# Performance work log

Hardware: AMD Instinct MI355X
Metric: run time of the kernel (lower is better)

The kernel has to match this reference:

```python
import jax, jax.numpy as jnp
import numpy as np
import math

B, S, D = 4, 512, 2048
NH, DEG = 8, 4            # chebyshev heads / degree
HD = D // NH              # 256
AH = 16                   # attention heads
AHD = D // AH             # 128
W = 512                   # local attention window
BASE_LR = 0.005

def rmsnorm(x, w, eps=1e-6):
    return x * jax.lax.rsqrt(jnp.mean(x * x, axis=-1, keepdims=True) + eps) * w

def cheby_rkv(xn, coeffs, momentum, gate, ema):
    # Chebyshev spectral read + EMA/TTT coefficient update (apply_cheby_rkv_v10)
    Bb, Ss, Dd = xn.shape
    u = xn.reshape(Bb, Ss, NH, HD)
    z = jnp.tanh(u.mean(-1))                       # (B,S,NH) in [-1,1]
    Ts = [jnp.ones_like(z), z]
    for _ in range(DEG - 2):
        Ts.append(2.0 * z * Ts[-1] - Ts[-2])       # Chebyshev recurrence
    T = jnp.stack(Ts[:DEG], axis=-1)               # (B,S,NH,DEG)
    out = jnp.einsum('bshk,bhkd->bshd', T, coeffs).reshape(Bb, Ss, Dd)
    grad = jnp.einsum('bshk,bshd->bhkd', T, u) / Ss
    mom = ema * momentum + (1.0 - ema) * grad
    coeffs_new = coeffs + BASE_LR * gate[:, :, None, None] * mom
    return out, coeffs_new, mom

def local_attention(q, k, v):
    # q,k,v: (B,H,S,hd); causal attention within a sliding window of W
    Bb, H, Ss, hd = q.shape
    nc = Ss // W
    q = q.reshape(Bb, H, nc, W, hd)
    k = k.reshape(Bb, H, nc, W, hd)
    v = v.reshape(Bb, H, nc, W, hd)
    kprev = jnp.concatenate([jnp.zeros_like(k[:, :, :1]), k[:, :, :-1]], axis=2)
    vprev = jnp.concatenate([jnp.zeros_like(v[:, :, :1]), v[:, :, :-1]], axis=2)
    kk = jnp.concatenate([kprev, k], axis=3)       # (B,H,nc,2W,hd)
    vv = jnp.concatenate([vprev, v], axis=3)
    qi = jnp.arange(W)
    kj = jnp.arange(2 * W)
    causal = (kj[None, :] - W) <= qi[:, None]      # (W,2W)
    chunk_ok = (jnp.arange(nc)[:, None, None] > 0) | (kj[None, None, :] >= W)
    mask = causal[None] & chunk_ok                 # (nc,W,2W)
    scores = jnp.einsum('bhnqd,bhnkd->bhnqk', q, kk) / math.sqrt(hd)
    scores = jnp.where(mask[None, None], scores, -1e9)
    attn = jax.nn.softmax(scores, axis=-1)
    o = jnp.einsum('bhnqk,bhnkd->bhnqd', attn, vv)
    return o.reshape(Bb, H, Ss, hd)

def _forward(x, w_in, wg1, bg1, wg2, bg2, wc1, bc1, wc2, bc2,
             wq, wk, wv, wo, w_nc, w_ns, w_fgv, w_np, w_out):
    Bb, Ss, Dd = x.shape
    xn = rmsnorm(x, w_in)
    x_mean = xn.mean(axis=1)                       # (B,D)
    # coeff init (cheby_state is None): MLP + spectral 1/(k+1) scaling
    h = jax.nn.silu(x_mean @ wc1 + bc1)
    coeff_raw = h @ wc2 + bc2
    kidx = jnp.arange(DEG, dtype=jnp.float32)
    spectral_scale = (0.1 / (kidx + 1.0)).reshape(1, 1, DEG, 1)
    coeffs = coeff_raw.reshape(Bb, NH, DEG, HD) * spectral_scale
    momentum = jnp.zeros_like(coeffs)
    # complexity gate (GatedComplexityPredictor)
    g = jax.nn.silu(x_mean @ wg1 + bg1)
    gate_global = jax.nn.sigmoid(g @ wg2 + bg2)    # (B,1)
    # EMA momentum schedule: total_tokens_seen = S after this call
    progress = min(Ss / 1e8, 1.0)
    ema = 0.7 + 0.5 * (0.9 - 0.7) * (1.0 + math.cos(progress * math.pi))
    cheby_out, coeffs, momentum = cheby_rkv(xn, coeffs, momentum, gate_global, ema)
    # SLR: windowed local attention, keys/values conditioned on cheby output
    kv_src = xn + cheby_out
    q = (xn @ wq).reshape(Bb, Ss, AH, AHD).transpose(0, 2, 1, 3)
    k = (kv_src @ wk).reshape(Bb, Ss, AH, AHD).transpose(0, 2, 1, 3)
    v = (kv_src @ wv).reshape(Bb, Ss, AH, AHD).transpose(0, 2, 1, 3)
    slr = local_attention(q, k, v).transpose(0, 2, 1, 3).reshape(Bb, Ss, Dd) @ wo
    # gated SwiGLU-style fusion of the two paths
    h1 = rmsnorm(cheby_out, w_nc)
    h2 = rmsnorm(slr, w_ns)
    gv = jnp.concatenate([h1, h2], axis=-1) @ w_fgv
    gate, value = gv[..., :Dd], gv[..., Dd:]
    fused = rmsnorm(jax.nn.silu(gate) * value, w_np)
    return x + fused @ w_out

def setup_inputs() -> dict:
    key = jax.random.key(0)
    ks = jax.random.split(key, 12)
    s = 0.02
    return {
        'x': jax.random.normal(ks[0], (B, S, D), jnp.float32),
        'w_in': jnp.ones((D,), jnp.float32),
        'wg1': jax.random.normal(ks[1], (D, D // 4), jnp.float32) * s,
        'bg1': jnp.zeros((D // 4,), jnp.float32),
        'wg2': jax.random.normal(ks[2], (D // 4, 1), jnp.float32) * s,
        'bg2': jnp.zeros((1,), jnp.float32),
        'wc1': jax.random.normal(ks[3], (D, D // 4), jnp.float32) * s,
        'bc1': jnp.zeros((D // 4,), jnp.float32),
        'wc2': jax.random.normal(ks[4], (D // 4, NH * DEG * HD), jnp.float32) * s,
        'bc2': jnp.zeros((NH * DEG * HD,), jnp.float32),
        'wq': jax.random.normal(ks[5], (D, D), jnp.float32) * s,
        'wk': jax.random.normal(ks[6], (D, D), jnp.float32) * s,
        'wv': jax.random.normal(ks[7], (D, D), jnp.float32) * s,
        'wo': jax.random.normal(ks[8], (D, D), jnp.float32) * s,
        'w_nc': jnp.ones((D,), jnp.float32),
        'w_ns': jnp.ones((D,), jnp.float32),
        'w_fgv': jax.random.normal(ks[9], (2 * D, 2 * D), jnp.float32) * s,
        'w_np': jnp.ones((D,), jnp.float32),
        'w_out': jax.random.normal(ks[10], (D, D), jnp.float32) * s,
    }

def reference(x, w_in, wg1, bg1, wg2, bg2, wc1, bc1, wc2, bc2,
              wq, wk, wv, wo, w_nc, w_ns, w_fgv, w_np, w_out):
    return _forward(x, w_in, wg1, bg1, wg2, bg2, wc1, bc1, wc2, bc2,
                    wq, wk, wv, wo, w_nc, w_ns, w_fgv, w_np, w_out)
```

## Files before the change

### kernel.cpp

```cpp
#include <hip/hip_runtime.h>
#include <hip/hip_bf16.h>
#include <math.h>

#define Bz 4
#define Sz 512
#define Dz 2048
#define NHz 8
#define DEGz 4
#define HDz 256
#define AHz 16
#define AHDz 128
#define SCALE_ATT 0.08838834764831845f

typedef __attribute__((ext_vector_type(8))) short short8;
typedef __attribute__((ext_vector_type(4))) float f32x4;

#define AS1 __attribute__((address_space(1)))
#define AS3 __attribute__((address_space(3)))

__device__ inline void gload16(const void* g, void* l) {
    __builtin_amdgcn_global_load_lds((const AS1 void*)g, (AS3 void*)l, 16, 0, 0);
}

struct GOp {
    const void* A; const void* B; void* C; const float* add;
    long long sAb, sAh, sBb, sBh, sCb, sCh;
    int K, lda, ldb, ldc, nbh, gx, gy, flags, tileEnd;
};
struct GArgs { int n; GOp op[6]; };

__global__ __launch_bounds__(256) void gemm_multi(GArgs ga) {
    __shared__ unsigned short As[2 * 128 * 32];
    __shared__ unsigned short Bs[2 * 128 * 32];

    int tid = blockIdx.x;
    int oi = 0;
    while (tid >= ga.op[oi].tileEnd) ++oi;
    GOp o = ga.op[oi];
    int local = tid - (oi ? ga.op[oi - 1].tileEnd : 0);
    int t = threadIdx.x;

    if (o.flags & 32) {
        const float* src = (const float*)o.A;
        __hip_bfloat16* dst = (__hip_bfloat16*)o.C;
        int ty = local / o.gx, tx = local - ty * o.gx;
        int k0 = ty * 32, n0 = tx * 32;
        float* tile = (float*)As;
        int c = t & 31, r8 = t >> 5;
#pragma unroll
        for (int p = 0; p < 4; ++p)
            tile[(r8 + p * 8) * 33 + c] = src[(long long)(k0 + r8 + p * 8) * o.lda + n0 + c];
        __syncthreads();
#pragma unroll
        for (int p = 0; p < 4; ++p)
            dst[(long long)(n0 + r8 + p * 8) * o.ldc + k0 + c] =
                __float2bfloat16(tile[c * 33 + r8 + p * 8]);
        return;
    }

    int perOp = o.gx * o.gy;
    int batch = local / perOp;
    int r3 = local - batch * perOp;
    int ty = r3 / o.gx;
    int tx = r3 - ty * o.gx;
    int row0 = ty * 128, col0 = tx * 128;

    if ((o.flags & 4) && (col0 > row0 + 127)) return;

    int zb = batch / o.nbh, zh = batch - zb * o.nbh;
    long long cb = (long long)zb * o.sCb + (long long)zh * o.sCh;

    int kEnd = o.K;
    if (o.flags & 8) { int ke = row0 + 128; kEnd = kEnd < ke ? kEnd : ke; }

    const unsigned short* Ab = (const unsigned short*)o.A + zb * o.sAb + zh * o.sAh;
    const unsigned short* Bb = (const unsigned short*)o.B + zb * o.sBb + zh * o.sBh;

    int w = t >> 6, l = t & 63;
    int lrow = l >> 2;
    int lchunk = (l & 3) * 8;

    const unsigned short* aP0 = Ab + (long long)(row0 + w * 16 + lrow) * o.lda + lchunk;
    const unsigned short* aP1 = aP0 + 64LL * o.lda;
    const unsigned short* bP0 = Bb + (long long)(col0 + w * 16 + lrow) * o.ldb + lchunk;
    const unsigned short* bP1 = bP0 + 64LL * o.ldb;
    unsigned short* aL0 = As + w * 512;
    unsigned short* aL1 = As + (w + 4) * 512;
    unsigned short* bL0 = Bs + w * 512;
    unsigned short* bL1 = Bs + (w + 4) * 512;

    int lm = l & 15, lq = l >> 4;
    int wr = (w >> 1) * 64, wc = (w & 1) * 64;

    f32x4 acc[4][4];
#pragma unroll
    for (int i = 0; i < 4; ++i)
#pragma unroll
        for (int j = 0; j < 4; ++j) acc[i][j] = (f32x4){0.f, 0.f, 0.f, 0.f};

    for (int k0 = 0; k0 < kEnd; k0 += 64) {
        gload16(aP0, aL0);
        gload16(aP1, aL1);
        gload16(bP0, bL0);
        gload16(bP1, bL1);
        gload16(aP0 + 32, aL0 + 4096);
        gload16(aP1 + 32, aL1 + 4096);
        gload16(bP0 + 32, bL0 + 4096);
        gload16(bP1 + 32, bL1 + 4096);
        aP0 += 64; aP1 += 64; bP0 += 64; bP1 += 64;
        __syncthreads();

#pragma unroll
        for (int h = 0; h < 2; ++h) {
            const unsigned short* Ah = As + h * 4096;
            const unsigned short* Bh = Bs + h * 4096;
            short8 af[4], bfr[4];
#pragma unroll
            for (int i = 0; i < 4; ++i)
                af[i] = *(const short8*)(Ah + (wr + i * 16 + lm) * 32 + lq * 8);
#pragma unroll
            for (int j = 0; j < 4; ++j)
                bfr[j] = *(const short8*)(Bh + (wc + j * 16 + lm) * 32 + lq * 8);
#pragma unroll
            for (int i = 0; i < 4; ++i)
#pragma unroll
                for (int j = 0; j < 4; ++j)
                    acc[i][j] = __builtin_amdgcn_mfma_f32_16x16x32_bf16(af[i], bfr[j], acc[i][j], 0, 0, 0);
        }
        __syncthreads();
    }

    if (o.flags & 1) {
        __hip_bfloat16* C = (__hip_bfloat16*)o.C;
#pragma unroll
        for (int i = 0; i < 4; ++i)
#pragma unroll
            for (int j = 0; j < 4; ++j)
#pragma unroll
                for (int r = 0; r < 4; ++r) {
                    int grow = row0 + wr + i * 16 + lq * 4 + r;
                    int gcol = col0 + wc + j * 16 + lm;
                    float v = acc[i][j][r];
                    if (o.flags & 4) v = (gcol > grow) ? -1e9f : v * SCALE_ATT;
                    C[cb + (long long)grow * o.ldc + gcol] = __float2bfloat16(v);
                }
    } else {
        float* C = (float*)o.C;
#pragma unroll
        for (int i = 0; i < 4; ++i)
#pragma unroll
            for (int j = 0; j < 4; ++j)
#pragma unroll
                for (int r = 0; r < 4; ++r) {
                    int grow = row0 + wr + i * 16 + lq * 4 + r;
                    int gcol = col0 + wc + j * 16 + lm;
                    float v = acc[i][j][r];
                    long long ci = cb + (long long)grow * o.ldc + gcol;
                    if (o.flags & 2) v += o.add[ci];
                    C[ci] = v;
                }
    }
}

__global__ __launch_bounds__(256) void rmsnorm_kernel(const float* __restrict__ x,
                                                      const float* __restrict__ w,
                                                      __hip_bfloat16* __restrict__ out) {
    long long base = (long long)blockIdx.x * Dz;
    int t = threadIdx.x;
    float v[8];
    float ss = 0.f;
#pragma unroll
    for (int p = 0; p < 8; ++p) { v[p] = x[base + t + p * 256]; ss += v[p] * v[p]; }
    __shared__ float red[256];
    red[t] = ss; __syncthreads();
    for (int s2 = 128; s2 > 0; s2 >>= 1) { if (t < s2) red[t] += red[t + s2]; __syncthreads(); }
    float sc = rsqrtf(red[0] / (float)Dz + 1e-6f);
#pragma unroll
    for (int p = 0; p < 8; ++p) { int c = t + p * 256; out[base + c] = __float2bfloat16(v[p] * sc * w[c]); }
}

__global__ __launch_bounds__(256) void xmean_p1(const __hip_bfloat16* __restrict__ xn,
                                                float* __restrict__ xmp) {
    int blk = blockIdx.x;
    int b = blk >> 6, sc = (blk >> 3) & 7, dc = blk & 7;
    int t = threadIdx.x;
    int d = dc * 256 + t;
    const __hip_bfloat16* p = xn + (long long)b * Sz * Dz + (long long)sc * 64 * Dz + d;
    float s = 0.f;
    for (int si = 0; si < 64; ++si) s += __bfloat162float(p[(long long)si * Dz]);
    xmp[(b * 8 + sc) * Dz + d] = s;
}

__global__ __launch_bounds__(256) void mlp1_kernel(const float* __restrict__ xmp,
                                                   const float* __restrict__ wc1,
                                                   const float* __restrict__ bc1,
                                                   float* __restrict__ h) {
    int blk = blockIdx.x;
    int b = blk >> 4, jb = blk & 15;
    int t = threadIdx.x;
    __shared__ float xs[Dz];
    __shared__ float red[8][32];
    const float* P = xmp + b * 8 * Dz;
#pragma unroll
    for (int p = 0; p < 8; ++p) {
        int d = t + p * 256;
        float s = 0.f;
#pragma unroll
        for (int q = 0; q < 8; ++q) s += P[q * Dz + d];
        xs[d] = s * (1.0f / (float)Sz);
    }
    __syncthreads();
    int j = jb * 32 + (t & 31), ksl = t >> 5;
    float s = 0.f;
    for (int k = ksl * 256; k < ksl * 256 + 256; ++k)
        s += xs[k] * wc1[(long long)k * 512 + j];
    red[ksl][t & 31] = s;
    __syncthreads();
    if (t < 32) {
        float tot = 0.f;
#pragma unroll
        for (int q = 0; q < 8; ++q) tot += red[q][t];
        tot += bc1[jb * 32 + t];
        h[b * 512 + jb * 32 + t] = tot / (1.0f + expf(-tot));
    }
}

__global__ __launch_bounds__(256) void coeffs_kernel(const float* __restrict__ h,
                                                     const float* __restrict__ wc2,
                                                     const float* __restrict__ bc2,
                                                     float* __restrict__ coeffs) {
    int blk = blockIdx.x;
    int b = blk >> 7, ib = blk & 127;
    int t = threadIdx.x;
    int i = ib * 64 + (t & 63), ksl = t >> 6;
    const float* hb = h + b * 512;
    float s = 0.f;
    for (int k = ksl * 128; k < ksl * 128 + 128; ++k)
        s += hb[k] * wc2[(long long)k * 8192 + i];
    __shared__ float red[4][64];
    red[ksl][t & 63] = s;
    __syncthreads();
    if (t < 64) {
        int ii = ib * 64 + t;
        float tot = red[0][t] + red[1][t] + red[2][t] + red[3][t] + bc2[ii];
        int kdeg = (ii >> 8) & 3;
        coeffs[b * 8192 + ii] = tot * (0.1f / (float)(kdeg + 1));
    }
}

__global__ __launch_bounds__(256) void cheby_kernel(const __hip_bfloat16* __restrict__ xn,
                                                    const float* __restrict__ coeffs,
                                                    __hip_bfloat16* __restrict__ cheby_out,
                                                    __hip_bfloat16* __restrict__ kv_src) {
    int bs = blockIdx.x;
    int b = bs >> 9;
    long long base = (long long)bs * Dz;
    int t = threadIdx.x;
    __shared__ float xrow[Dz];
    __shared__ float hsum[NHz][33];
    __shared__ float T[NHz][4];
#pragma unroll
    for (int p = 0; p < 8; ++p) xrow[t + p * 256] = __bfloat162float(xn[base + t + p * 256]);
    __syncthreads();
    int hh = t >> 5, lane = t & 31;
    float s = 0.f;
#pragma unroll
    for (int q = 0; q < 8; ++q) s += xrow[hh * HDz + lane + q * 32];
    hsum[hh][lane] = s;
    __syncthreads();
    if (t < NHz) {
        float tot = 0.f;
        for (int l2 = 0; l2 < 32; ++l2) tot += hsum[t][l2];
        float z = tanhf(tot / (float)HDz);
        float t2 = 2.f * z * z - 1.f;
        T[t][0] = 1.f; T[t][1] = z; T[t][2] = t2; T[t][3] = 2.f * z * t2 - z;
    }
    __syncthreads();
    const float* cbp = coeffs + (long long)b * (NHz * DEGz * HDz);
#pragma unroll
    for (int p = 0; p < 8; ++p) {
        int e = t + p * 256;
        int hd = e >> 8;
        int d = e & (HDz - 1);
        const float* ch = cbp + hd * (DEGz * HDz) + d;
        float co = T[hd][0] * ch[0] + T[hd][1] * ch[HDz] + T[hd][2] * ch[2 * HDz] + T[hd][3] * ch[3 * HDz];
        cheby_out[base + e] = __float2bfloat16(co);
        kv_src[base + e] = __float2bfloat16(xrow[e] + co);
    }
}

__global__ __launch_bounds__(128) void softmax_kernel(__hip_bfloat16* __restrict__ sc) {
    long long rid = blockIdx.x;
    int i = (int)(rid & (Sz - 1));
    long long base = rid * Sz;
    int t = threadIdx.x;
    float vals[4];
    float mx = -1e30f;
#pragma unroll
    for (int p = 0; p < 4; ++p) {
        int j = t + p * 128;
        float v = __bfloat162float(sc[base + j]);
        if (j > i) v = -1e9f;
        vals[p] = v;
        mx = fmaxf(mx, v);
    }
    __shared__ float red[128];
    red[t] = mx; __syncthreads();
    for (int s2 = 64; s2 > 0; s2 >>= 1) { if (t < s2) red[t] = fmaxf(red[t], red[t + s2]); __syncthreads(); }
    mx = red[0]; __syncthreads();
    float sum = 0.f;
#pragma unroll
    for (int p = 0; p < 4; ++p) { vals[p] = __expf(vals[p] - mx); sum += vals[p]; }
    red[t] = sum; __syncthreads();
    for (int s2 = 64; s2 > 0; s2 >>= 1) { if (t < s2) red[t] += red[t + s2]; __syncthreads(); }
    float inv = 1.0f / red[0];
#pragma unroll
    for (int p = 0; p < 4; ++p) sc[base + t + p * 128] = __float2bfloat16(vals[p] * inv);
}

__global__ __launch_bounds__(256) void hcat_kernel(const __hip_bfloat16* __restrict__ cheby,
                                                   const __hip_bfloat16* __restrict__ slr,
                                                   const float* __restrict__ w_nc,
                                                   const float* __restrict__ w_ns,
                                                   __hip_bfloat16* __restrict__ hcat) {
    long long row = blockIdx.x;
    const __hip_bfloat16* c = cheby + row * Dz;
    const __hip_bfloat16* sl = slr + row * Dz;
    __hip_bfloat16* o = hcat + row * (2 * Dz);
    int t = threadIdx.x;
    float v1[8], v2[8];
    float ss1 = 0.f, ss2 = 0.f;
#pragma unroll
    for (int p = 0; p < 8; ++p) {
        v1[p] = __bfloat162float(c[t + p * 256]);  ss1 += v1[p] * v1[p];
        v2[p] = __bfloat162float(sl[t + p * 256]); ss2 += v2[p] * v2[p];
    }
    __shared__ float red[256];
    red[t] = ss1; __syncthreads();
    for (int s2 = 128; s2 > 0; s2 >>= 1) { if (t < s2) red[t] += red[t + s2]; __syncthreads(); }
    float sc1 = rsqrtf(red[0] / (float)Dz + 1e-6f);
    __syncthreads();
    red[t] = ss2; __syncthreads();
    for (int s2 = 128; s2 > 0; s2 >>= 1) { if (t < s2) red[t] += red[t + s2]; __syncthreads(); }
    float sc2 = rsqrtf(red[0] / (float)Dz + 1e-6f);
#pragma unroll
    for (int p = 0; p < 8; ++p) {
        int cx = t + p * 256;
        o[cx] = __float2bfloat16(v1[p] * sc1 * w_nc[cx]);
        o[Dz + cx] = __float2bfloat16(v2[p] * sc2 * w_ns[cx]);
    }
}

__global__ __launch_bounds__(256) void fusedgate_kernel(const __hip_bfloat16* __restrict__ gv,
                                                        const float* __restrict__ w_np,
                                                        __hip_bfloat16* __restrict__ fused) {
    long long row = blockIdx.x;
    const __hip_bfloat16* g = gv + row * (2 * Dz);
    __hip_bfloat16* o = fused + row * Dz;
    int t = threadIdx.x;
    float f[8];
    float ss = 0.f;
#pragma unroll
    for (int p = 0; p < 8; ++p) {
        float ga = __bfloat162float(g[t + p * 256]);
        float va = __bfloat162float(g[Dz + t + p * 256]);
        float sv = ga / (1.0f + expf(-ga)) * va;
        f[p] = sv; ss += sv * sv;
    }
    __shared__ float red[256];
    red[t] = ss; __syncthreads();
    for (int s2 = 128; s2 > 0; s2 >>= 1) { if (t < s2) red[t] += red[t + s2]; __syncthreads(); }
    float sc = rsqrtf(red[0] / (float)Dz + 1e-6f);
#pragma unroll
    for (int p = 0; p < 8; ++p) { int cx = t + p * 256; o[cx] = __float2bfloat16(f[p] * sc * w_np[cx]); }
}

static GOp gop(const void* A, const void* B, void* C, const float* add,
               int K, int lda, int ldb, int ldc, int nbh, int nb, int gx, int gy,
               long long sAb, long long sAh, long long sBb, long long sBh,
               long long sCb, long long sCh, int flags) {
    GOp o;
    o.A = A; o.B = B; o.C = C; o.add = add;
    o.sAb = sAb; o.sAh = sAh; o.sBb = sBb; o.sBh = sBh; o.sCb = sCb; o.sCh = sCh;
    o.K = K; o.lda = lda; o.ldb = ldb; o.ldc = ldc; o.nbh = nbh;
    o.gx = gx; o.gy = gy; o.flags = flags;
    o.tileEnd = (flags & 32) ? gx * gy : nb * gx * gy;
    return o;
}

static void launch_multi(hipStream_t st, GOp* ops, int n) {
    GArgs ga; ga.n = n;
    int acc = 0;
    for (int i = 0; i < n; ++i) { acc += ops[i].tileEnd; ga.op[i] = ops[i]; ga.op[i].tileEnd = acc; }
    hipLaunchKernelGGL(gemm_multi, dim3(acc), dim3(256), 0, st, ga);
}

extern "C" void kernel_launch(void* const* d_in, const int* in_sizes, int n_in,
                              void* d_out, int out_size, void* d_ws, size_t ws_size,
                              hipStream_t stream) {
    const float* x     = (const float*)d_in[0];
    const float* w_in  = (const float*)d_in[1];
    const float* wc1   = (const float*)d_in[6];
    const float* bc1   = (const float*)d_in[7];
    const float* wc2   = (const float*)d_in[8];
    const float* bc2   = (const float*)d_in[9];
    const float* wq    = (const float*)d_in[10];
    const float* wk    = (const float*)d_in[11];
    const float* wv    = (const float*)d_in[12];
    const float* wo    = (const float*)d_in[13];
    const float* w_nc  = (const float*)d_in[14];
    const float* w_ns  = (const float*)d_in[15];
    const float* w_fgv = (const float*)d_in[16];
    const float* w_np  = (const float*)d_in[17];
    const float* w_out = (const float*)d_in[18];
    float* out = (float*)d_out;

    const size_t MB = 1ull << 20;
    char* W = (char*)d_ws;
    __hip_bfloat16* xn_bf    = (__hip_bfloat16*)(W + 0 * MB);
    __hip_bfloat16* kv_bf    = (__hip_bfloat16*)(W + 8 * MB);
    __hip_bfloat16* cheby_bf = (__hip_bfloat16*)(W + 16 * MB);
    __hip_bfloat16* q_bf     = (__hip_bfloat16*)(W + 24 * MB);
    __hip_bfloat16* k_bf     = (__hip_bfloat16*)(W + 32 * MB);
    __hip_bfloat16* vT_bf    = (__hip_bfloat16*)(W + 40 * MB);
    __hip_bfloat16* o_bf     = (__hip_bfloat16*)(W + 48 * MB);
    __hip_bfloat16* scores   = (__hip_bfloat16*)(W + 56 * MB);
    __hip_bfloat16* wq_t     = (__hip_bfloat16*)(W + 88 * MB);
    __hip_bfloat16* wk_t     = (__hip_bfloat16*)(W + 96 * MB);
    __hip_bfloat16* wv_t     = (__hip_bfloat16*)(W + 104 * MB);
    __hip_bfloat16* wo_t     = (__hip_bfloat16*)(W + 112 * MB);
    __hip_bfloat16* wout_t   = (__hip_bfloat16*)(W + 120 * MB);
    __hip_bfloat16* wfgv_t   = (__hip_bfloat16*)(W + 56 * MB);
    __hip_bfloat16* slr_bf   = (__hip_bfloat16*)(W + 0 * MB);
    __hip_bfloat16* hcat_bf  = (__hip_bfloat16*)(W + 24 * MB);
    __hip_bfloat16* gv_bf    = (__hip_bfloat16*)(W + 40 * MB);
    __hip_bfloat16* fused_bf = (__hip_bfloat16*)(W + 8 * MB);
    float* xmp   = (float*)(W + 128 * MB);
    float* hbuf  = xmp + 65536;
    float* cbuf  = hbuf + 2048;

    const int BS = Bz * Sz;
    const long long SD = (long long)Sz * Dz;
    const long long SS = (long long)Sz * Sz;

    {
        GOp ops[5];
        const float* srcs[5] = {wq, wk, wv, wo, w_out};
        __hip_bfloat16* dsts[5] = {wq_t, wk_t, wv_t, wo_t, wout_t};
        for (int i = 0; i < 5; ++i)
            ops[i] = gop(srcs[i], nullptr, dsts[i], nullptr, Dz, Dz, 0, Dz,
                         1, 1, 64, 64, 0, 0, 0, 0, 0, 0, 32);
        launch_multi(stream, ops, 5);
    }
    hipLaunchKernelGGL(rmsnorm_kernel, dim3(BS), dim3(256), 0, stream, x, w_in, xn_bf);
    hipLaunchKernelGGL(xmean_p1, dim3(256), dim3(256), 0, stream, xn_bf, xmp);
    hipLaunchKernelGGL(mlp1_kernel, dim3(64), dim3(256), 0, stream, xmp, wc1, bc1, hbuf);
    hipLaunchKernelGGL(coeffs_kernel, dim3(512), dim3(256), 0, stream, hbuf, wc2, bc2, cbuf);
    hipLaunchKernelGGL(cheby_kernel, dim3(BS), dim3(256), 0, stream, xn_bf, cbuf, cheby_bf, kv_bf);
    {
        GOp ops[3];
        ops[0] = gop(xn_bf, wq_t, q_bf, nullptr, Dz, Dz, Dz, Dz, 1, 1, 16, 16,
                     0, 0, 0, 0, 0, 0, 1);
        ops[1] = gop(kv_bf, wk_t, k_bf, nullptr, Dz, Dz, Dz, Dz, 1, 1, 16, 16,
                     0, 0, 0, 0, 0, 0, 1);
        ops[2] = gop(wv_t, kv_bf, vT_bf, nullptr, Dz, Dz, Dz, Sz, 1, Bz, 4, 16,
                     0, 0, SD, 0, (long long)Dz * Sz, 0, 1);
        launch_multi(stream, ops, 3);
    }
    {
        GOp op = gop(q_bf, k_bf, scores, nullptr, AHDz, Dz, Dz, Sz, AHz, Bz * AHz, 4, 4,
                     SD, AHDz, SD, AHDz, (long long)AHz * SS, SS, 1 | 4);
        launch_multi(stream, &op, 1);
    }
    hipLaunchKernelGGL(softmax_kernel, dim3(Bz * AHz * Sz), dim3(128), 0, stream, scores);
    {
        GOp op = gop(scores, vT_bf, o_bf, nullptr, Sz, Sz, Sz, Dz, AHz, Bz * AHz, 1, 4,
                     (long long)AHz * SS, SS, (long long)Dz * Sz, 128LL * Sz,
                     SD, 128, 1 | 8);
        launch_multi(stream, &op, 1);
    }
    {
        GOp ops[2];
        ops[0] = gop(o_bf, wo_t, slr_bf, nullptr, Dz, Dz, Dz, Dz, 1, 1, 16, 16,
                     0, 0, 0, 0, 0, 0, 1);
        ops[1] = gop(w_fgv, nullptr, wfgv_t, nullptr, 2 * Dz, 2 * Dz, 0, 2 * Dz,
                     1, 1, 128, 128, 0, 0, 0, 0, 0, 0, 32);
        launch_multi(stream, ops, 2);
    }
    hipLaunchKernelGGL(hcat_kernel, dim3(BS), dim3(256), 0, stream, cheby_bf, slr_bf, w_nc, w_ns, hcat_bf);
    {
        GOp op = gop(hcat_bf, wfgv_t, gv_bf, nullptr, 2 * Dz, 2 * Dz, 2 * Dz, 2 * Dz,
                     1, 1, 32, 16, 0, 0, 0, 0, 0, 0, 1);
        launch_multi(stream, &op, 1);
    }
    hipLaunchKernelGGL(fusedgate_kernel, dim3(BS), dim3(256), 0, stream, gv_bf, w_np, fused_bf);
    {
        GOp op = gop(fused_bf, wout_t, out, x, Dz, Dz, Dz, Dz, 1, 1, 16, 16,
                     0, 0, 0, 0, 0, 0, 2);
        launch_multi(stream, &op, 1);
    }
}
```

Baseline: 623.0 us.

## Add 128x256-tile 512-thread double-buffered GEMM kernel for large projections

Adds a new GEMM kernel that uses 128x256 output tiles with 8 waves per block, double-buffered LDS filled by direct global-to-LDS loads, and loads split across the two MFMA phases. The Q/K/V, output-projection, fgv and final GEMMs switch to it with halved grid widths. The w_fgv transpose is split out of the wo launch because the new kernel has no transpose path. Larger tiles raise data reuse and overlap loads with compute, but the grids get fewer blocks and each block needs much more LDS, which can lower occupancy.

```diff
diff --git a/kernel.cpp b/kernel.cpp
--- a/kernel.cpp
+++ b/kernel.cpp
@@ -154,6 +154,159 @@
                 for (int r = 0; r < 4; ++r) {
                     int grow = row0 + wr + i * 16 + lq * 4 + r;
                     int gcol = col0 + wc + j * 16 + lm;
+                    float v = acc[i][j][r];
+                    long long ci = cb + (long long)grow * o.ldc + gcol;
+                    if (o.flags & 2) v += o.add[ci];
+                    C[ci] = v;
+                }
+    }
+}
+
+__global__ __launch_bounds__(512) void gemm_dp(GArgs ga) {
+    __shared__ unsigned short As[2][128 * 64];
+    __shared__ unsigned short Bs[2][256 * 64];
+
+    int tid = blockIdx.x;
+    int oi = 0;
+    while (tid >= ga.op[oi].tileEnd) ++oi;
+    GOp o = ga.op[oi];
+    int local = tid - (oi ? ga.op[oi - 1].tileEnd : 0);
+    int t = threadIdx.x;
+
+    int perOp = o.gx * o.gy;
+    int batch = local / perOp;
+    int r3 = local - batch * perOp;
+    int ty = r3 / o.gx, tx = r3 - ty * o.gx;
+    int row0 = ty * 128, col0 = tx * 256;
+
+    int zb = batch / o.nbh, zh = batch - zb * o.nbh;
+    long long cb = (long long)zb * o.sCb + (long long)zh * o.sCh;
+
+    const unsigned short* Ab = (const unsigned short*)o.A + zb * o.sAb + zh * o.sAh;
+    const unsigned short* Bb = (const unsigned short*)o.B + zb * o.sBb + zh * o.sBh;
+
+    int w = t >> 6, l = t & 63;
+    int srow = w * 8 + (l >> 3);
+    int scol = ((l & 7) ^ (l >> 3)) << 3;
+
+    const unsigned short* aS0 = Ab + (long long)(row0 + srow) * o.lda + scol;
+    const unsigned short* aS1 = Ab + (long long)(row0 + 64 + srow) * o.lda + scol;
+    const unsigned short* bS0 = Bb + (long long)(col0 + srow) * o.ldb + scol;
+    const unsigned short* bS1 = Bb + (long long)(col0 + 64 + srow) * o.ldb + scol;
+    const unsigned short* bS2 = Bb + (long long)(col0 + 128 + srow) * o.ldb + scol;
+    const unsigned short* bS3 = Bb + (long long)(col0 + 192 + srow) * o.ldb + scol;
+
+    int wofs = w * 512;
+
+    gload16(aS0, &As[0][wofs]);
+    gload16(aS1, &As[0][4096 + wofs]);
+    gload16(bS0, &Bs[0][wofs]);
+    gload16(bS1, &Bs[0][4096 + wofs]);
+    gload16(bS2, &Bs[0][8192 + wofs]);
+    gload16(bS3, &Bs[0][12288 + wofs]);
+    aS0 += 64; aS1 += 64; bS0 += 64; bS1 += 64; bS2 += 64; bS3 += 64;
+
+    int lm = l & 15, lq = l >> 4;
+    int wr = w >> 2, wc = w & 3;
+    int c0 = ((lq) ^ (lm & 7)) << 3;
+    int c1 = ((4 + lq) ^ (lm & 7)) << 3;
+
+    f32x4 acc[4][4];
+#pragma unroll
+    for (int i = 0; i < 4; ++i)
+#pragma unroll
+        for (int j = 0; j < 4; ++j) acc[i][j] = (f32x4){0.f, 0.f, 0.f, 0.f};
+
+    int nkt = o.K >> 6;
+    for (int kt = 0; kt < nkt; ++kt) {
+        unsigned short* Ac = &As[kt & 1][0];
+        unsigned short* Bc = &Bs[kt & 1][0];
+        unsigned short* An = &As[(kt & 1) ^ 1][0];
+        unsigned short* Bn = &Bs[(kt & 1) ^ 1][0];
+
+        if (kt + 1 < nkt) {
+            gload16(aS0, An + wofs);
+            gload16(aS1, An + 4096 + wofs);
+            gload16(bS0, Bn + wofs);
+            asm volatile("s_waitcnt vmcnt(3)" ::: "memory");
+        } else {
+            asm volatile("s_waitcnt vmcnt(0)" ::: "memory");
+        }
+        __builtin_amdgcn_s_barrier();
+        __builtin_amdgcn_sched_barrier(0);
+
+        short8 a0[2][2], b0[4][2];
+#pragma unroll
+        for (int mi = 0; mi < 2; ++mi) {
+            const unsigned short* ar = Ac + (wr * 64 + mi * 16 + lm) * 64;
+            a0[mi][0] = *(const short8*)(ar + c0);
+            a0[mi][1] = *(const short8*)(ar + c1);
+        }
+#pragma unroll
+        for (int nj = 0; nj < 4; ++nj) {
+            const unsigned short* br = Bc + (wc * 64 + nj * 16 + lm) * 64;
+            b0[nj][0] = *(const short8*)(br + c0);
+            b0[nj][1] = *(const short8*)(br + c1);
+        }
+        __builtin_amdgcn_s_setprio(1);
+#pragma unroll
+        for (int kh = 0; kh < 2; ++kh)
+#pragma unroll
+            for (int mi = 0; mi < 2; ++mi)
+#pragma unroll
+                for (int nj = 0; nj < 4; ++nj)
+                    acc[mi][nj] = __builtin_amdgcn_mfma_f32_16x16x32_bf16(a0[mi][kh], b0[nj][kh], acc[mi][nj], 0, 0, 0);
+        __builtin_amdgcn_s_setprio(0);
+
+        if (kt + 1 < nkt) {
+            gload16(bS1, Bn + 4096 + wofs);
+            gload16(bS2, Bn + 8192 + wofs);
+            gload16(bS3, Bn + 12288 + wofs);
+            aS0 += 64; aS1 += 64; bS0 += 64; bS1 += 64; bS2 += 64; bS3 += 64;
+        }
+        short8 a1[2][2];
+#pragma unroll
+        for (int mi = 0; mi < 2; ++mi) {
+            const unsigned short* ar = Ac + (wr * 64 + (mi + 2) * 16 + lm) * 64;
+            a1[mi][0] = *(const short8*)(ar + c0);
+            a1[mi][1] = *(const short8*)(ar + c1);
+        }
+        __builtin_amdgcn_s_setprio(1);
+#pragma unroll
+        for (int kh = 0; kh < 2; ++kh)
+#pragma unroll
+            for (int mi = 0; mi < 2; ++mi)
+#pragma unroll
+                for (int nj = 0; nj < 4; ++nj)
+                    acc[mi + 2][nj] = __builtin_amdgcn_mfma_f32_16x16x32_bf16(a1[mi][kh], b0[nj][kh], acc[mi + 2][nj], 0, 0, 0);
+        __builtin_amdgcn_s_setprio(0);
+        __builtin_amdgcn_sched_barrier(0);
+        __builtin_amdgcn_s_barrier();
+        __builtin_amdgcn_sched_barrier(0);
+    }
+
+    if (o.flags & 1) {
+        __hip_bfloat16* C = (__hip_bfloat16*)o.C;
+#pragma unroll
+        for (int i = 0; i < 4; ++i)
+#pragma unroll
+            for (int j = 0; j < 4; ++j)
+#pragma unroll
+                for (int r = 0; r < 4; ++r) {
+                    int grow = row0 + wr * 64 + i * 16 + lq * 4 + r;
+                    int gcol = col0 + wc * 64 + j * 16 + lm;
+                    C[cb + (long long)grow * o.ldc + gcol] = __float2bfloat16(acc[i][j][r]);
+                }
+    } else {
+        float* C = (float*)o.C;
+#pragma unroll
+        for (int i = 0; i < 4; ++i)
+#pragma unroll
+            for (int j = 0; j < 4; ++j)
+#pragma unroll
+                for (int r = 0; r < 4; ++r) {
+                    int grow = row0 + wr * 64 + i * 16 + lq * 4 + r;
+                    int gcol = col0 + wc * 64 + j * 16 + lm;
                     float v = acc[i][j][r];
                     long long ci = cb + (long long)grow * o.ldc + gcol;
                     if (o.flags & 2) v += o.add[ci];
@@ -393,6 +546,13 @@
     int acc = 0;
     for (int i = 0; i < n; ++i) { acc += ops[i].tileEnd; ga.op[i] = ops[i]; ga.op[i].tileEnd = acc; }
     hipLaunchKernelGGL(gemm_multi, dim3(acc), dim3(256), 0, st, ga);
+}
+
+static void launch_dp(hipStream_t st, GOp* ops, int n) {
+    GArgs ga; ga.n = n;
+    int acc = 0;
+    for (int i = 0; i < n; ++i) { acc += ops[i].tileEnd; ga.op[i] = ops[i]; ga.op[i].tileEnd = acc; }
+    hipLaunchKernelGGL(gemm_dp, dim3(acc), dim3(512), 0, st, ga);
 }
 
 extern "C" void kernel_launch(void* const* d_in, const int* in_sizes, int n_in,
@@ -459,13 +619,13 @@
     hipLaunchKernelGGL(cheby_kernel, dim3(BS), dim3(256), 0, stream, xn_bf, cbuf, cheby_bf, kv_bf);
     {
         GOp ops[3];
-        ops[0] = gop(xn_bf, wq_t, q_bf, nullptr, Dz, Dz, Dz, Dz, 1, 1, 16, 16,
+        ops[0] = gop(xn_bf, wq_t, q_bf, nullptr, Dz, Dz, Dz, Dz, 1, 1, 8, 16,
                      0, 0, 0, 0, 0, 0, 1);
-        ops[1] = gop(kv_bf, wk_t, k_bf, nullptr, Dz, Dz, Dz, Dz, 1, 1, 16, 16,
+        ops[1] = gop(kv_bf, wk_t, k_bf, nullptr, Dz, Dz, Dz, Dz, 1, 1, 8, 16,
                      0, 0, 0, 0, 0, 0, 1);
-        ops[2] = gop(wv_t, kv_bf, vT_bf, nullptr, Dz, Dz, Dz, Sz, 1, Bz, 4, 16,
+        ops[2] = gop(wv_t, kv_bf, vT_bf, nullptr, Dz, Dz, Dz, Sz, 1, Bz, 2, 16,
                      0, 0, SD, 0, (long long)Dz * Sz, 0, 1);
-        launch_multi(stream, ops, 3);
+        launch_dp(stream, ops, 3);
     }
     {
         GOp op = gop(q_bf, k_bf, scores, nullptr, AHDz, Dz, Dz, Sz, AHz, Bz * AHz, 4, 4,
@@ -480,23 +640,25 @@
         launch_multi(stream, &op, 1);
     }
     {
-        GOp ops[2];
-        ops[0] = gop(o_bf, wo_t, slr_bf, nullptr, Dz, Dz, Dz, Dz, 1, 1, 16, 16,
+        GOp op = gop(w_fgv, nullptr, wfgv_t, nullptr, 2 * Dz, 2 * Dz, 0, 2 * Dz,
+                     1, 1, 128, 128, 0, 0, 0, 0, 0, 0, 32);
+        launch_multi(stream, &op, 1);
+    }
+    {
+        GOp op = gop(o_bf, wo_t, slr_bf, nullptr, Dz, Dz, Dz, Dz, 1, 1, 8, 16,
                      0, 0, 0, 0, 0, 0, 1);
-        ops[1] = gop(w_fgv, nullptr, wfgv_t, nullptr, 2 * Dz, 2 * Dz, 0, 2 * Dz,
-                     1, 1, 128, 128, 0, 0, 0, 0, 0, 0, 32);
-        launch_multi(stream, ops, 2);
+        launch_dp(stream, &op, 1);
     }
     hipLaunchKernelGGL(hcat_kernel, dim3(BS), dim3(256), 0, stream, cheby_bf, slr_bf, w_nc, w_ns, hcat_bf);
     {
         GOp op = gop(hcat_bf, wfgv_t, gv_bf, nullptr, 2 * Dz, 2 * Dz, 2 * Dz, 2 * Dz,
-                     1, 1, 32, 16, 0, 0, 0, 0, 0, 0, 1);
-        launch_multi(stream, &op, 1);
+                     1, 1, 16, 16, 0, 0, 0, 0, 0, 0, 1);
+        launch_dp(stream, &op, 1);
     }
     hipLaunchKernelGGL(fusedgate_kernel, dim3(BS), dim3(256), 0, stream, gv_bf, w_np, fused_bf);
     {
-        GOp op = gop(fused_bf, wout_t, out, x, Dz, Dz, Dz, Dz, 1, 1, 16, 16,
+        GOp op = gop(fused_bf, wout_t, out, x, Dz, Dz, Dz, Dz, 1, 1, 8, 16,
                      0, 0, 0, 0, 0, 0, 2);
-        launch_multi(stream, &op, 1);
-    }
-}
+        launch_dp(stream, &op, 1);
+    }
+}
```

Result: no change. 616.9 us (-1.0%).
